# Kernel tuning notes

Hardware: AMD Instinct MI355X
Metric: run time of the kernel (lower is better)

## Reference

```python
import jax, jax.numpy as jnp
import numpy as np

B, N = 8, 4096
SEM_IN, SEM_OUT = 128, 13
INS_IN, INS_OUT = 128, 5
K = 30


def conv1x1(x, W, b):
    # x: [B, Cin, N], W: [Cout, Cin] -> [B, Cout, N]
    return jnp.einsum('oc,bcn->bon', W, x) + b[None, :, None]


def setup_inputs() -> dict:
    key = jax.random.key(0)
    ks = jax.random.split(key, 6)
    rn = lambda i, shape: jax.random.normal(ks[i], shape, dtype=jnp.float32)
    return {
        'f_sem': rn(0, (B, SEM_IN, N)),
        'f_ins': rn(1, (B, INS_IN, N)),
        'W_adapt': rn(2, (INS_IN, SEM_IN)) * 0.05,
        'b_adapt': jnp.zeros((INS_IN,), jnp.float32),
        'gamma_adapt': jnp.ones((INS_IN,), jnp.float32),
        'beta_adapt': jnp.zeros((INS_IN,), jnp.float32),
        'W_ins': rn(3, (INS_OUT, INS_IN)) * 0.05,
        'b_ins': jnp.zeros((INS_OUT,), jnp.float32),
        'W_sem': rn(4, (SEM_OUT, SEM_IN)) * 0.05,
        'b_sem': jnp.zeros((SEM_OUT,), jnp.float32),
    }


def reference(f_sem, f_ins, W_adapt, b_adapt, gamma_adapt, beta_adapt,
              W_ins, b_ins, W_sem, b_sem):
    # adaptation MLP: Conv1d(1x1) -> eval-mode BN (per-channel affine) -> ReLU
    adapted = conv1x1(f_sem, W_adapt, b_adapt)
    adapted = jax.nn.relu(adapted * gamma_adapt[None, :, None] + beta_adapt[None, :, None])
    f_sins = f_ins + adapted                       # [B, INS_IN, N]
    e_ins = conv1x1(f_sins, W_ins, b_ins)          # [B, INS_OUT, N]; Dropout=identity (eval)

    # k_nearest_neighbors(e_ins, e_ins, K): squared euclidean + top-k smallest
    sq = jnp.sum(e_ins * e_ins, axis=1)            # [B, N]
    dots = jnp.einsum('bcn,bcm->bnm', e_ins, e_ins)  # [B, N, N]
    dist = sq[:, :, None] - 2.0 * dots + sq[:, None, :]
    _, nn_idx = jax.lax.top_k(-dist, K)            # [B, N, K] indices of K nearest

    # index2points gather: [B, C, N, K]
    k_f_sem = jax.vmap(lambda f, i: f[:, i])(f_sem, nn_idx)
    f_isem = jnp.max(k_f_sem, axis=3)              # max over neighbors -> [B, C, N]

    p_sem = conv1x1(f_isem, W_sem, b_sem)          # [B, SEM_OUT, N]
    return p_sem, e_ins
```

## Files before the change

### kernel.cpp

```cpp
#include <hip/hip_runtime.h>
#include <stdint.h>

#define B_ 8
#define N_ 4096
#define C_ 128
#define OSEM 13
#define OINS 5
#define KNN 30
#define NSC 32
#define ROWS 4

typedef unsigned short u16;
typedef unsigned int u32;
typedef unsigned long long u64;

__device__ __forceinline__ float bf2f(u16 v) {
  u32 u = ((u32)v) << 16;
  return __uint_as_float(u);
}
__device__ __forceinline__ u16 f2bf(float f) {
  u32 u = __float_as_uint(f);
  u32 r = (u + 0x7FFFu + ((u >> 16) & 1u)) >> 16;
  return (u16)r;
}
__device__ __forceinline__ u32 monof(float d) {
  u32 u = __float_as_uint(d);
  return (u & 0x80000000u) ? ~u : (u | 0x80000000u);
}
__device__ __forceinline__ float unmonof(u32 p) {
  u32 u = (p & 0x80000000u) ? (p & 0x7FFFFFFFu) : ~p;
  return __uint_as_float(u);
}
__device__ __forceinline__ u64 monod(double d) {
  u64 u = (u64)__double_as_longlong(d);
  return (u & 0x8000000000000000ull) ? ~u : (u | 0x8000000000000000ull);
}
__device__ __forceinline__ int mbcnt64(u64 m) {
  return __builtin_amdgcn_mbcnt_hi((u32)(m >> 32),
                                   __builtin_amdgcn_mbcnt_lo((u32)m, 0));
}
__device__ __forceinline__ float rflf(float x) {
  return __uint_as_float(
      (u32)__builtin_amdgcn_readfirstlane((int)__float_as_uint(x)));
}

template <int M>
__device__ __forceinline__ float ldv(const void* p, size_t i) {
  if (M == 0) return bf2f(((const u16*)p)[i]);
  return ((const float*)p)[i];
}
template <int M>
__device__ __forceinline__ double ldvd(const void* p, size_t i) {
  return (double)ldv<M>(p, i);
}
template <int M>
__device__ __forceinline__ void stv(void* p, size_t i, float v) {
  if (M == 0) ((u16*)p)[i] = f2bf(v);
  else ((float*)p)[i] = v;
}
template <int M>
__device__ __forceinline__ void ld8(const void* p, size_t i, float* o) {
  if (M == 0) {
    uint4 u = *(const uint4*)((const u16*)p + i);
    o[0] = __uint_as_float(u.x << 16); o[1] = __uint_as_float(u.x & 0xFFFF0000u);
    o[2] = __uint_as_float(u.y << 16); o[3] = __uint_as_float(u.y & 0xFFFF0000u);
    o[4] = __uint_as_float(u.z << 16); o[5] = __uint_as_float(u.z & 0xFFFF0000u);
    o[6] = __uint_as_float(u.w << 16); o[7] = __uint_as_float(u.w & 0xFFFF0000u);
  } else {
    const float4* f = (const float4*)((const float*)p + i);
    float4 a = f[0], b = f[1];
    o[0] = a.x; o[1] = a.y; o[2] = a.z; o[3] = a.w;
    o[4] = b.x; o[5] = b.y; o[6] = b.z; o[7] = b.w;
  }
}

template <typename T>
__device__ __forceinline__ void transpose_body(const void* src_, void* dst_,
                                               char* tsm, int b, int c0,
                                               int n0) {
  T* t = (T*)tsm;
  const T* src0 = (const T*)src_;
  T* dst0 = (T*)dst_;
  int tid = threadIdx.x, j = tid & 63, i0 = tid >> 6;
  const T* src = src0 + (size_t)(b * C_ + c0) * N_ + n0;
#pragma unroll
  for (int k = 0; k < 16; ++k) {
    int i = k * 4 + i0;
    t[i * 65 + j] = src[(size_t)i * N_ + j];
  }
  __syncthreads();
  T* dst = dst0 + ((size_t)b * N_ + n0) * C_ + c0;
#pragma unroll
  for (int k = 0; k < 16; ++k) {
    int nl = k * 4 + i0;
    dst[(size_t)nl * C_ + j] = t[j * 65 + nl];
  }
}

template <int M>
__device__ void fused_body(const void* fsem, const void* fins, const void* Wad,
                           const void* bad, const void* gad, const void* bead,
                           const void* Wins, const void* bins,
                           float* __restrict__ q32, double* __restrict__ q64,
                           void* oute, char* smem, int b, int n0) {
  double* xs = (double*)smem;
  double* wt = (double*)(smem + 20480);
  float* fsh = (float*)smem;
  float* fsl = (float*)(smem + 32768);

  int tid = threadIdx.x, tx = tid & 7, ty = tid >> 3;

  double acc[4][8];
#pragma unroll
  for (int i = 0; i < 4; ++i)
#pragma unroll
    for (int j = 0; j < 8; ++j) acc[i][j] = 0.0;

  for (int kk = 0; kk < 128; kk += 32) {
    __syncthreads();
    {
      int r = tid >> 3, c8 = tid & 7;
      float v[8];
      ld8<M>(fsem, (size_t)(b * C_ + kk + r) * N_ + n0 + c8 * 8, v);
#pragma unroll
      for (int j = 0; j < 8; ++j) xs[r * 80 + c8 * 10 + j] = (double)v[j];
    }
#pragma unroll
    for (int it = 0; it < 16; ++it) {
      int f = it * 256 + tid;
      int k = f >> 7, c = f & 127;
      wt[k * 128 + c] = ldvd<M>(Wad, (size_t)c * C_ + kk + k);
    }
    __syncthreads();
#pragma unroll 2
    for (int k = 0; k < 32; ++k) {
      double xv[8], wv[4];
#pragma unroll
      for (int j = 0; j < 8; ++j) xv[j] = xs[k * 80 + tx * 10 + j];
#pragma unroll
      for (int i = 0; i < 4; ++i) wv[i] = wt[k * 128 + ty * 4 + i];
#pragma unroll
      for (int i = 0; i < 4; ++i)
#pragma unroll
        for (int j = 0; j < 8; ++j) acc[i][j] = fma(wv[i], xv[j], acc[i][j]);
    }
  }

#pragma unroll
  for (int i = 0; i < 4; ++i) {
    int c = ty * 4 + i;
    double ba = ldvd<M>(bad, c), ga = ldvd<M>(gad, c), be = ldvd<M>(bead, c);
    float ff[8];
    ld8<M>(fins, (size_t)(b * C_ + c) * N_ + n0 + tx * 8, ff);
#pragma unroll
    for (int j = 0; j < 8; ++j) {
      double a = acc[i][j] + ba;
      double h = a * ga + be;
      h = h > 0.0 ? h : 0.0;
      acc[i][j] = (double)ff[j] + h;
    }
  }
  __syncthreads();

#pragma unroll
  for (int i = 0; i < 4; ++i) {
    int c = ty * 4 + i;
#pragma unroll
    for (int j = 0; j < 8; ++j) {
      double fs = acc[i][j];
      float hi = (float)fs;
      fsh[c * 64 + tx * 8 + j] = hi;
      fsl[c * 64 + tx * 8 + j] = (float)(fs - (double)hi);
    }
  }
  __syncthreads();
  if (tid < 64) {
    int n = n0 + tid;
    double e[5] = {0.0, 0.0, 0.0, 0.0, 0.0};
#pragma unroll 4
    for (int c = 0; c < 128; ++c) {
      double fs = (double)fsh[c * 64 + tid] + (double)fsl[c * 64 + tid];
#pragma unroll
      for (int o = 0; o < 5; ++o)
        e[o] = fma(ldvd<M>(Wins, (size_t)o * C_ + c), fs, e[o]);
    }
    double sq = 0.0;
#pragma unroll
    for (int o = 0; o < 5; ++o) {
      e[o] = e[o] + ldvd<M>(bins, o);
      sq = fma(e[o], e[o], sq);
      stv<M>(oute, (size_t)(b * OINS + o) * N_ + n, (float)e[o]);
    }
    size_t row = (size_t)b * N_ + n;
    float* qp = q32 + row * 8;
    qp[0] = (float)e[0]; qp[1] = (float)e[1]; qp[2] = (float)e[2];
    qp[3] = (float)e[3]; qp[4] = (float)e[4]; qp[5] = (float)sq;
    qp[6] = 0.f; qp[7] = 0.f;
    double* qd = q64 + row * 8;
    qd[0] = e[0]; qd[1] = e[1]; qd[2] = e[2]; qd[3] = e[3]; qd[4] = e[4];
    qd[5] = sq; qd[6] = 0.0; qd[7] = 0.0;
  }
}

__global__ __launch_bounds__(256) void k_prep(
    const void* fsem, const void* fins, const void* Wad, const void* bad,
    const void* gad, const void* bead, const void* Wins, const void* bins,
    float* q32, double* q64, void* oute_bf, void* oute_f, void* fT,
    int useFT0, int useFT1, u32* flag) {
  __shared__ __align__(16) char smem[65536];
  __shared__ int sred[4];

  int tid = threadIdx.x;
  int csn = 0;
  {
    const u16* p = (const u16*)fsem;
#pragma unroll
    for (int i = 0; i < 4; ++i) {
      u16 v = p[2 * (tid * 4 + i)];
      u32 e = (v >> 7) & 0xFF;
      csn += (e >= 0x60 && e <= 0x9F) ? 1 : 0;
    }
#pragma unroll
    for (int s = 1; s < 64; s <<= 1) csn += __shfl_xor(csn, s, 64);
    if ((tid & 63) == 0) sred[tid >> 6] = csn;
  }
  __syncthreads();
  u32 fl = ((sred[0] + sred[1] + sred[2] + sred[3]) >= 614) ? 0u : 1u;

  int bx = blockIdx.x;
  if (bx == 0 && tid == 0) flag[0] = fl;

  if (bx < 512) {
    int b = bx >> 6, n0 = (bx & 63) * 64;
    if (fl == 0)
      fused_body<0>(fsem, fins, Wad, bad, gad, bead, Wins, bins, q32, q64,
                    oute_bf, smem, b, n0);
    else
      fused_body<1>(fsem, fins, Wad, bad, gad, bead, Wins, bins, q32, q64,
                    oute_f, smem, b, n0);
  } else {
    int idx = bx - 512;
    int n0 = (idx & 63) * 64, c0 = ((idx >> 6) & 1) * 64, b = idx >> 7;
    if (fl == 0) {
      if (!useFT0) return;
      transpose_body<u16>(fsem, fT, smem, b, c0, n0);
    } else {
      if (!useFT1) return;
      transpose_body<float>(fsem, fT, smem, b, c0, n0);
    }
  }
}

template <int M>
__device__ __forceinline__ void gather_pass(int b, const u32* __restrict__ fp,
                                            const void* fT, int c0,
                                            float* mx) {
#pragma unroll 3
  for (int k = 0; k < KNN; ++k) {
    int id = (int)fp[k];
    if (M == 0) {
      uint2 v = *(const uint2*)((const u16*)fT + (size_t)(b * N_ + id) * C_ + c0);
      mx[0] = fmaxf(mx[0], __uint_as_float(v.x << 16));
      mx[1] = fmaxf(mx[1], __uint_as_float(v.x & 0xFFFF0000u));
      mx[2] = fmaxf(mx[2], __uint_as_float(v.y << 16));
      mx[3] = fmaxf(mx[3], __uint_as_float(v.y & 0xFFFF0000u));
    } else {
      float4 v = *(const float4*)((const float*)fT + (size_t)(b * N_ + id) * C_ + c0);
      mx[0] = fmaxf(mx[0], v.x);
      mx[1] = fmaxf(mx[1], v.y);
      mx[2] = fmaxf(mx[2], v.z);
      mx[3] = fmaxf(mx[3], v.w);
    }
  }
}

template <int M>
__device__ __forceinline__ void gather_proj(int b, int n, const u32* fin,
                                            const void* fsem,
                                            const float* wsm,
                                            const float* bsm, float* fls,
                                            void* outv, int lane) {
  float mx0 = -__builtin_inff(), mx1 = -__builtin_inff();
  int c0 = lane * 2;
  size_t base = ((size_t)b * C_ + c0) * N_;
#pragma unroll 2
  for (int k = 0; k < KNN; ++k) {
    int id = (int)fin[k];
    mx0 = fmaxf(mx0, ldv<M>(fsem, base + id));
    mx1 = fmaxf(mx1, ldv<M>(fsem, base + N_ + id));
  }
  int g0 = c0 >> 5, cc0 = c0 & 31;
  fls[g0 * 33 + cc0] = mx0;
  fls[g0 * 33 + cc0 + 1] = mx1;
  if (lane < 52) {
    int o = lane >> 2, g = lane & 3;
    const float* wr = &wsm[(o * 4 + g) * 33];
    const float* fr = &fls[g * 33];
    float s = 0.f;
#pragma unroll
    for (int c = 0; c < 32; ++c) s = fmaf(wr[c], fr[c], s);
    s += __shfl_xor(s, 1, 64);
    s += __shfl_xor(s, 2, 64);
    if (g == 0) stv<M>(outv, ((size_t)b * OSEM + o) * N_ + n, s + bsm[o]);
  }
}

__global__ __launch_bounds__(256) void k_knn_out(
    const u32* flag, const float* __restrict__ q32,
    const double* __restrict__ q64, const void* fsem, const void* fT,
    int useFT0, int useFT1, const void* Wsem, const void* bsem, void* outv) {
  __shared__ u64 bufs[4][ROWS][128];
  __shared__ u32 idq[4][NSC];
  __shared__ u32 fin[4][ROWS][32];
  __shared__ float bsm[16];

  int tid = threadIdx.x, wid = tid >> 6, lane = tid & 63;
  u32 fl = *flag;
  int useFT = fl == 0 ? useFT0 : useFT1;

  int gw = blockIdx.x * 4 + wid;
  int b = gw >> 10;
  int r0 = (gw & 1023) * ROWS;
  const float* qb = q32 + (((size_t)b) << 12) * 8;
  u64(*buf)[128] = bufs[wid];

#pragma unroll
  for (int i = 0; i < 2 * ROWS; ++i) bufs[wid][0][i * 64 + lane] = ~0ull;

  float er2[ROWS][5], t[ROWS];
  int cnt[ROWS];
#pragma unroll
  for (int r = 0; r < ROWS; ++r) {
    const float* qr = qb + (size_t)(r0 + r) * 8;
    er2[r][0] = -2.f * qr[0]; er2[r][1] = -2.f * qr[1];
    er2[r][2] = -2.f * qr[2]; er2[r][3] = -2.f * qr[3];
    er2[r][4] = -2.f * qr[4];
    cnt[r] = 0;
  }

  auto rank_compress = [&](u64* bufr) -> float {
    u64 k0 = bufr[lane], k1 = bufr[lane + 64];
    int f0 = 0, f1 = 0;
#pragma unroll 4
    for (int j = 0; j < 64; ++j) {
      ulonglong2 kk = *(const ulonglong2*)&bufr[2 * j];
      f0 += (kk.x < k0) ? 1 : 0;
      f0 += (kk.y < k0) ? 1 : 0;
      f1 += (kk.x < k1) ? 1 : 0;
      f1 += (kk.y < k1) ? 1 : 0;
    }
    bool h31 = (f0 == 31) || (f1 == 31);
    u64 who = __ballot(h31);
    u32 pk = (f0 == 31) ? (u32)(k0 >> 32) : (u32)(k1 >> 32);
    int src = (int)(__ffsll((long long)who) - 1);
    pk = (u32)__shfl((int)pk, src, 64);
    bufr[64 + lane] = ~0ull;
    if (f0 < 64) bufr[f0] = k0;
    if (f1 < 64) bufr[f1] = k1;
    return unmonof(pk);
  };

  float minv[ROWS];
#pragma unroll
  for (int r = 0; r < ROWS; ++r) minv[r] = __builtin_inff();
  int pcur = gw & 31;
  float4 A0, A1;
  float2 B0, B1;
  {
    const float* g = qb + (size_t)pcur * 1024 + lane * 8;
    A0 = *(const float4*)(g);       B0 = *(const float2*)(g + 4);
    A1 = *(const float4*)(g + 512); B1 = *(const float2*)(g + 516);
  }
#pragma unroll 1
  for (int it = 0; it < 32; ++it) {
#pragma unroll
    for (int r = 0; r < ROWS; ++r) {
      float dd = B0.y;
      dd = fmaf(er2[r][0], A0.x, dd);
      dd = fmaf(er2[r][1], A0.y, dd);
      dd = fmaf(er2[r][2], A0.z, dd);
      dd = fmaf(er2[r][3], A0.w, dd);
      dd = fmaf(er2[r][4], B0.x, dd);
      float ee = B1.y;
      ee = fmaf(er2[r][0], A1.x, ee);
      ee = fmaf(er2[r][1], A1.y, ee);
      ee = fmaf(er2[r][2], A1.z, ee);
      ee = fmaf(er2[r][3], A1.w, ee);
      ee = fmaf(er2[r][4], B1.x, ee);
      minv[r] = fminf(minv[r], fminf(dd, ee));
    }
    pcur = (pcur + 1) & 31;
    {
      const float* g = qb + (size_t)pcur * 1024 + lane * 8;
      A0 = *(const float4*)(g);       B0 = *(const float2*)(g + 4);
      A1 = *(const float4*)(g + 512); B1 = *(const float2*)(g + 516);
    }
  }

  {
    u64 KM[ROWS];
    int fr2[ROWS];
#pragma unroll
    for (int r = 0; r < ROWS; ++r) {
      KM[r] = ((u64)monof(minv[r]) << 6) | (u32)lane;
      buf[r][lane] = KM[r];
      fr2[r] = 0;
    }
#pragma unroll 2
    for (int j = 0; j < 32; ++j) {
#pragma unroll
      for (int r = 0; r < ROWS; ++r) {
        ulonglong2 kk = *(const ulonglong2*)&buf[r][2 * j];
        fr2[r] += (kk.x < KM[r]) ? 1 : 0;
        fr2[r] += (kk.y < KM[r]) ? 1 : 0;
      }
    }
#pragma unroll
    for (int r = 0; r < ROWS; ++r) {
      bool h = (fr2[r] == 31);
      u64 who = __ballot(h);
      int src = (int)(__ffsll((long long)who) - 1);
      u32 pk = (u32)(KM[r] >> 6);
      pk = (u32)__shfl((int)pk, src, 64);
      t[r] = rflf(unmonof(pk));
      buf[r][lane] = ~0ull;
    }
  }

  pcur = gw & 31;
  {
    const float* g = qb + (size_t)pcur * 1024 + lane * 8;
    A0 = *(const float4*)(g);       B0 = *(const float2*)(g + 4);
    A1 = *(const float4*)(g + 512); B1 = *(const float2*)(g + 516);
  }
#pragma unroll 1
  for (int it = 0; it < 32; ++it) {
    int mb = pcur * 128;
    float d0[ROWS], d1[ROWS];
    u64 h0[ROWS], h1[ROWS];
#pragma unroll
    for (int r = 0; r < ROWS; ++r) {
      float dd = B0.y;
      dd = fmaf(er2[r][0], A0.x, dd);
      dd = fmaf(er2[r][1], A0.y, dd);
      dd = fmaf(er2[r][2], A0.z, dd);
      dd = fmaf(er2[r][3], A0.w, dd);
      dd = fmaf(er2[r][4], B0.x, dd);
      d0[r] = dd;
      float ee = B1.y;
      ee = fmaf(er2[r][0], A1.x, ee);
      ee = fmaf(er2[r][1], A1.y, ee);
      ee = fmaf(er2[r][2], A1.z, ee);
      ee = fmaf(er2[r][3], A1.w, ee);
      ee = fmaf(er2[r][4], B1.x, ee);
      d1[r] = ee;
      h0[r] = __ballot(dd <= t[r]);
      h1[r] = __ballot(ee <= t[r]);
    }
    pcur = (pcur + 1) & 31;
    {
      const float* g = qb + (size_t)pcur * 1024 + lane * 8;
      A0 = *(const float4*)(g);       B0 = *(const float2*)(g + 4);
      A1 = *(const float4*)(g + 512); B1 = *(const float2*)(g + 516);
    }
#pragma unroll
    for (int r = 0; r < ROWS; ++r) {
      u64 a = h0[r], c = h1[r];
      int m0 = mb + lane, m1 = mb + 64 + lane;
      if (a | c) {
        int ha = __popcll(a), hc = __popcll(c);
        if (cnt[r] + ha + hc <= 128) {
          int oa = mbcnt64(a), oc = ha + mbcnt64(c);
          if (d0[r] <= t[r])
            buf[r][cnt[r] + oa] = ((u64)monof(d0[r]) << 32) | (u32)m0;
          if (d1[r] <= t[r])
            buf[r][cnt[r] + oc] = ((u64)monof(d1[r]) << 32) | (u32)m1;
          cnt[r] += ha + hc;
        } else {
          if (cnt[r] + ha > 128) {
            t[r] = rflf(rank_compress(&buf[r][0]));
            cnt[r] = 64;
            a = __ballot(d0[r] <= t[r]);
            ha = __popcll(a);
          }
          if (ha) {
            int oa = mbcnt64(a);
            if (d0[r] <= t[r])
              buf[r][cnt[r] + oa] = ((u64)monof(d0[r]) << 32) | (u32)m0;
            cnt[r] += ha;
          }
          u64 c2 = __ballot(d1[r] <= t[r]);
          int hc2 = __popcll(c2);
          if (cnt[r] + hc2 > 128) {
            t[r] = rflf(rank_compress(&buf[r][0]));
            cnt[r] = 64;
            c2 = __ballot(d1[r] <= t[r]);
            hc2 = __popcll(c2);
          }
          if (hc2) {
            int oc = mbcnt64(c2);
            if (d1[r] <= t[r])
              buf[r][cnt[r] + oc] = ((u64)monof(d1[r]) << 32) | (u32)m1;
            cnt[r] += hc2;
          }
        }
      }
    }
  }

  const double* qdb = q64 + (((size_t)b) << 12) * 8;
  {
    u64 K0[ROWS], K1[ROWS];
    int f0[ROWS], f1[ROWS];
    int cmax = 0;
#pragma unroll
    for (int r = 0; r < ROWS; ++r) {
      K0[r] = buf[r][lane];
      K1[r] = buf[r][lane + 64];
      f0[r] = 0; f1[r] = 0;
      cmax = cnt[r] > cmax ? cnt[r] : cmax;
    }
    int JJ = (cmax + 1) >> 1;
#pragma unroll 2
    for (int j = 0; j < JJ; ++j) {
#pragma unroll
      for (int r = 0; r < ROWS; ++r) {
        ulonglong2 kk = *(const ulonglong2*)&buf[r][2 * j];
        f0[r] += (kk.x < K0[r]) ? 1 : 0;
        f0[r] += (kk.y < K0[r]) ? 1 : 0;
        f1[r] += (kk.x < K1[r]) ? 1 : 0;
        f1[r] += (kk.y < K1[r]) ? 1 : 0;
      }
    }
#pragma unroll 1
    for (int r = 0; r < ROWS; ++r) {
      if (f0[r] < NSC) idq[wid][f0[r]] = (u32)K0[r] & (N_ - 1);
      if (f1[r] < NSC) idq[wid][f1[r]] = (u32)K1[r] & (N_ - 1);

      const double* qdr = qdb + (size_t)(r0 + r) * 8;
      double D0 = qdr[0], D1 = qdr[1], D2 = qdr[2], D3 = qdr[3], D4 = qdr[4],
             DS = qdr[5];
      u64 key = ~0ull;
      u32 myid = 0;
      if (lane < NSC) {
        myid = idq[wid][lane];
        const double* qm = qdb + (size_t)myid * 8;
        double dot = D0 * qm[0];
        dot = fma(D1, qm[1], dot);
        dot = fma(D2, qm[2], dot);
        dot = fma(D3, qm[3], dot);
        dot = fma(D4, qm[4], dot);
        double dd = (DS - 2.0 * dot) + qm[5];
        key = (monod(dd) & ~0xFFFull) | myid;
      }
      buf[r][lane] = key;
      int rank = 0;
#pragma unroll
      for (int j = 0; j < NSC / 2; ++j) {
        ulonglong2 kk = *(const ulonglong2*)&buf[r][2 * j];
        rank += (kk.x < key) ? 1 : 0;
        rank += (kk.y < key) ? 1 : 0;
      }
      if (lane < NSC && rank < KNN) fin[wid][r][rank] = myid;
    }
  }

  __syncthreads();
  float* wsm = (float*)&bufs[0][0][0];
  float* flsb = (float*)&bufs[0][0][0] + 1728;
  for (int i = tid; i < 13 * 128; i += 256) {
    int o = i >> 7, cc = i & 127;
    wsm[(o * 4 + (cc >> 5)) * 33 + (cc & 31)] =
        (fl == 0) ? ldv<0>(Wsem, i) : ldv<1>(Wsem, i);
  }
  if (tid < OSEM) bsm[tid] = (fl == 0) ? ldv<0>(bsem, tid) : ldv<1>(bsem, tid);
  __syncthreads();

  if (useFT) {
    int h = lane >> 5, l5 = lane & 31, c0 = l5 * 4;
#pragma unroll 1
    for (int pass = 0; pass < 2; ++pass) {
      int r = pass * 2 + h;
      float mx[4] = {-__builtin_inff(), -__builtin_inff(), -__builtin_inff(),
                     -__builtin_inff()};
      if (fl == 0)
        gather_pass<0>(b, &fin[wid][r][0], fT, c0, mx);
      else
        gather_pass<1>(b, &fin[wid][r][0], fT, c0, mx);
      float* fr = flsb + (wid * ROWS + r) * 136 + (c0 >> 5) * 33 + (c0 & 31);
      fr[0] = mx[0]; fr[1] = mx[1]; fr[2] = mx[2]; fr[3] = mx[3];
    }
    if (lane < 52) {
      int o = lane >> 2, g = lane & 3;
      const float* wr = &wsm[(o * 4 + g) * 33];
      const float* p0 = flsb + (wid * ROWS + 0) * 136 + g * 33;
      const float* p1 = flsb + (wid * ROWS + 1) * 136 + g * 33;
      const float* p2 = flsb + (wid * ROWS + 2) * 136 + g * 33;
      const float* p3 = flsb + (wid * ROWS + 3) * 136 + g * 33;
      float s0 = 0.f, s1 = 0.f, s2 = 0.f, s3 = 0.f;
#pragma unroll
      for (int c = 0; c < 32; ++c) {
        float w = wr[c];
        s0 = fmaf(w, p0[c], s0);
        s1 = fmaf(w, p1[c], s1);
        s2 = fmaf(w, p2[c], s2);
        s3 = fmaf(w, p3[c], s3);
      }
      s0 += __shfl_xor(s0, 1, 64); s0 += __shfl_xor(s0, 2, 64);
      s1 += __shfl_xor(s1, 1, 64); s1 += __shfl_xor(s1, 2, 64);
      s2 += __shfl_xor(s2, 1, 64); s2 += __shfl_xor(s2, 2, 64);
      s3 += __shfl_xor(s3, 1, 64); s3 += __shfl_xor(s3, 2, 64);
      if (g == 0) {
        size_t ob = (size_t)b * OSEM + o;
        if (fl == 0) {
          stv<0>(outv, ob * N_ + r0 + 0, s0 + bsm[o]);
          stv<0>(outv, ob * N_ + r0 + 1, s1 + bsm[o]);
          stv<0>(outv, ob * N_ + r0 + 2, s2 + bsm[o]);
          stv<0>(outv, ob * N_ + r0 + 3, s3 + bsm[o]);
        } else {
          stv<1>(outv, ob * N_ + r0 + 0, s0 + bsm[o]);
          stv<1>(outv, ob * N_ + r0 + 1, s1 + bsm[o]);
          stv<1>(outv, ob * N_ + r0 + 2, s2 + bsm[o]);
          stv<1>(outv, ob * N_ + r0 + 3, s3 + bsm[o]);
        }
      }
    }
  } else {
    float* fls = flsb + (wid * ROWS) * 136;
#pragma unroll 1
    for (int r = 0; r < ROWS; ++r) {
      if (fl == 0)
        gather_proj<0>(b, r0 + r, &fin[wid][r][0], fsem, wsm, bsm, fls, outv,
                       lane);
      else
        gather_proj<1>(b, r0 + r, &fin[wid][r][0], fsem, wsm, bsm, fls, outv,
                       lane);
    }
  }
}

extern "C" void kernel_launch(void* const* d_in, const int* in_sizes, int n_in,
                              void* d_out, int out_size, void* d_ws,
                              size_t ws_size, hipStream_t stream) {
  (void)in_sizes; (void)n_in; (void)out_size;
  const void* fsem = d_in[0];
  const void* fins = d_in[1];
  const void* Wad = d_in[2];
  const void* bad = d_in[3];
  const void* gad = d_in[4];
  const void* bead = d_in[5];
  const void* Wins = d_in[6];
  const void* bins = d_in[7];
  const void* Wsem = d_in[8];
  const void* bsem = d_in[9];

  char* ws = (char*)d_ws;
  u32* flag = (u32*)ws;
  float* q32 = (float*)(ws + (1 << 20));
  double* q64 = (double*)(ws + (2 << 20));
  void* fT = (void*)(ws + (4 << 20));
  int useFT0 = (ws_size >= (size_t)(13 << 20)) ? 1 : 0;
  int useFT1 = (ws_size >= (size_t)(21 << 20)) ? 1 : 0;

  void* oute_bf = (void*)((u16*)d_out + (size_t)B_ * OSEM * N_);
  void* oute_f32 = (void*)((float*)d_out + (size_t)B_ * OSEM * N_);

  k_prep<<<dim3(1536), 256, 0, stream>>>(fsem, fins, Wad, bad, gad, bead,
                                         Wins, bins, q32, q64, oute_bf,
                                         oute_f32, fT, useFT0, useFT1, flag);
  k_knn_out<<<dim3(2048), 256, 0, stream>>>(flag, q32, q64, fsem, fT, useFT0,
                                            useFT1, Wsem, bsem, d_out);
}
```

Baseline: 259.6 us.

## Halve prep tile width, store adapt operands as float, parallelize e_ins projection

The fused prep kernel now processes 32 points per block instead of 64, doubling the fused-block count. The adapt-conv operands are staged in shared memory as float instead of double, and the accumulator shrinks from 4x8 to 2x8 doubles per thread. Shared memory drops from 64KB to about 34KB, which should raise occupancy and cut LDS traffic. The 5-output e_ins projection is split across 160 threads, one output channel each, instead of 64 threads computing all five. The cost is more blocks, an extra barrier, and more redundant weight loads per block.

```diff
diff --git a/kernel.cpp b/kernel.cpp
--- a/kernel.cpp
+++ b/kernel.cpp
@@ -73,6 +73,19 @@
     o[4] = b.x; o[5] = b.y; o[6] = b.z; o[7] = b.w;
   }
 }
+template <int M>
+__device__ __forceinline__ void ld4(const void* p, size_t i, float* o) {
+  if (M == 0) {
+    uint2 u = *(const uint2*)((const u16*)p + i);
+    o[0] = __uint_as_float(u.x << 16); o[1] = __uint_as_float(u.x & 0xFFFF0000u);
+    o[2] = __uint_as_float(u.y << 16); o[3] = __uint_as_float(u.y & 0xFFFF0000u);
+  } else {
+    float4 v = *(const float4*)((const float*)p + i);
+    o[0] = v.x; o[1] = v.y; o[2] = v.z; o[3] = v.w;
+  }
+}
+
+#define PREP_SMEM 34048
 
 template <typename T>
 __device__ __forceinline__ void transpose_body(const void* src_, void* dst_,
@@ -103,52 +116,55 @@
                            const void* Wins, const void* bins,
                            float* __restrict__ q32, double* __restrict__ q64,
                            void* oute, char* smem, int b, int n0) {
-  double* xs = (double*)smem;
-  double* wt = (double*)(smem + 20480);
+  float* wtf = (float*)smem;
+  float* xsf = (float*)(smem + 16384);
   float* fsh = (float*)smem;
-  float* fsl = (float*)(smem + 32768);
-
-  int tid = threadIdx.x, tx = tid & 7, ty = tid >> 3;
-
-  double acc[4][8];
-#pragma unroll
-  for (int i = 0; i < 4; ++i)
+  float* fsl = (float*)(smem + 16384);
+  double* est = (double*)(smem + 32768);
+
+  int tid = threadIdx.x, tx = tid & 3, ty = tid >> 2;
+
+  double acc[2][8];
+#pragma unroll
+  for (int i = 0; i < 2; ++i)
 #pragma unroll
     for (int j = 0; j < 8; ++j) acc[i][j] = 0.0;
 
   for (int kk = 0; kk < 128; kk += 32) {
     __syncthreads();
     {
-      int r = tid >> 3, c8 = tid & 7;
-      float v[8];
-      ld8<M>(fsem, (size_t)(b * C_ + kk + r) * N_ + n0 + c8 * 8, v);
-#pragma unroll
-      for (int j = 0; j < 8; ++j) xs[r * 80 + c8 * 10 + j] = (double)v[j];
+      int idx = tid * 4;
+      int k = idx >> 5, nn = idx & 31;
+      float v[4];
+      ld4<M>(fsem, (size_t)(b * C_ + kk + k) * N_ + n0 + nn, v);
+      xsf[k * 32 + nn] = v[0]; xsf[k * 32 + nn + 1] = v[1];
+      xsf[k * 32 + nn + 2] = v[2]; xsf[k * 32 + nn + 3] = v[3];
     }
 #pragma unroll
     for (int it = 0; it < 16; ++it) {
       int f = it * 256 + tid;
       int k = f >> 7, c = f & 127;
-      wt[k * 128 + c] = ldvd<M>(Wad, (size_t)c * C_ + kk + k);
+      wtf[k * 128 + c] = ldv<M>(Wad, (size_t)c * C_ + kk + k);
     }
     __syncthreads();
 #pragma unroll 2
     for (int k = 0; k < 32; ++k) {
-      double xv[8], wv[4];
-#pragma unroll
-      for (int j = 0; j < 8; ++j) xv[j] = xs[k * 80 + tx * 10 + j];
-#pragma unroll
-      for (int i = 0; i < 4; ++i) wv[i] = wt[k * 128 + ty * 4 + i];
-#pragma unroll
-      for (int i = 0; i < 4; ++i)
-#pragma unroll
-        for (int j = 0; j < 8; ++j) acc[i][j] = fma(wv[i], xv[j], acc[i][j]);
-    }
-  }
-
-#pragma unroll
-  for (int i = 0; i < 4; ++i) {
-    int c = ty * 4 + i;
+      float xvf[8], wvf[2];
+#pragma unroll
+      for (int j = 0; j < 8; ++j) xvf[j] = xsf[k * 32 + tx * 8 + j];
+#pragma unroll
+      for (int i = 0; i < 2; ++i) wvf[i] = wtf[k * 128 + ty * 2 + i];
+#pragma unroll
+      for (int i = 0; i < 2; ++i)
+#pragma unroll
+        for (int j = 0; j < 8; ++j)
+          acc[i][j] = fma((double)wvf[i], (double)xvf[j], acc[i][j]);
+    }
+  }
+
+#pragma unroll
+  for (int i = 0; i < 2; ++i) {
+    int c = ty * 2 + i;
     double ba = ldvd<M>(bad, c), ga = ldvd<M>(gad, c), be = ldvd<M>(bead, c);
     float ff[8];
     ld8<M>(fins, (size_t)(b * C_ + c) * N_ + n0 + tx * 8, ff);
@@ -163,31 +179,39 @@
   __syncthreads();
 
 #pragma unroll
-  for (int i = 0; i < 4; ++i) {
-    int c = ty * 4 + i;
+  for (int i = 0; i < 2; ++i) {
+    int c = ty * 2 + i;
 #pragma unroll
     for (int j = 0; j < 8; ++j) {
       double fs = acc[i][j];
       float hi = (float)fs;
-      fsh[c * 64 + tx * 8 + j] = hi;
-      fsl[c * 64 + tx * 8 + j] = (float)(fs - (double)hi);
+      fsh[c * 32 + tx * 8 + j] = hi;
+      fsl[c * 32 + tx * 8 + j] = (float)(fs - (double)hi);
     }
   }
   __syncthreads();
-  if (tid < 64) {
+  {
+    int lane = tid & 63;
+    int slot = (tid >> 6) * 2 + (lane >> 5);
+    int n = lane & 31;
+    if (slot < 5) {
+      double e = 0.0;
+#pragma unroll 4
+      for (int c = 0; c < 128; ++c) {
+        double fs = (double)fsh[c * 32 + n] + (double)fsl[c * 32 + n];
+        e = fma(ldvd<M>(Wins, (size_t)slot * C_ + c), fs, e);
+      }
+      est[slot * 32 + n] = e;
+    }
+  }
+  __syncthreads();
+  if (tid < 32) {
     int n = n0 + tid;
-    double e[5] = {0.0, 0.0, 0.0, 0.0, 0.0};
-#pragma unroll 4
-    for (int c = 0; c < 128; ++c) {
-      double fs = (double)fsh[c * 64 + tid] + (double)fsl[c * 64 + tid];
-#pragma unroll
-      for (int o = 0; o < 5; ++o)
-        e[o] = fma(ldvd<M>(Wins, (size_t)o * C_ + c), fs, e[o]);
-    }
+    double e[5];
     double sq = 0.0;
 #pragma unroll
     for (int o = 0; o < 5; ++o) {
-      e[o] = e[o] + ldvd<M>(bins, o);
+      e[o] = est[o * 32 + tid] + ldvd<M>(bins, o);
       sq = fma(e[o], e[o], sq);
       stv<M>(oute, (size_t)(b * OINS + o) * N_ + n, (float)e[o]);
     }
@@ -207,7 +231,7 @@
     const void* gad, const void* bead, const void* Wins, const void* bins,
     float* q32, double* q64, void* oute_bf, void* oute_f, void* fT,
     int useFT0, int useFT1, u32* flag) {
-  __shared__ __align__(16) char smem[65536];
+  __shared__ __align__(16) char smem[PREP_SMEM];
   __shared__ int sred[4];
 
   int tid = threadIdx.x;
@@ -230,8 +254,8 @@
   int bx = blockIdx.x;
   if (bx == 0 && tid == 0) flag[0] = fl;
 
-  if (bx < 512) {
-    int b = bx >> 6, n0 = (bx & 63) * 64;
+  if (bx < 1024) {
+    int b = bx >> 7, n0 = (bx & 127) * 32;
     if (fl == 0)
       fused_body<0>(fsem, fins, Wad, bad, gad, bead, Wins, bins, q32, q64,
                     oute_bf, smem, b, n0);
@@ -239,7 +263,7 @@
       fused_body<1>(fsem, fins, Wad, bad, gad, bead, Wins, bins, q32, q64,
                     oute_f, smem, b, n0);
   } else {
-    int idx = bx - 512;
+    int idx = bx - 1024;
     int n0 = (idx & 63) * 64, c0 = ((idx >> 6) & 1) * 64, b = idx >> 7;
     if (fl == 0) {
       if (!useFT0) return;
@@ -665,7 +689,7 @@
   void* oute_bf = (void*)((u16*)d_out + (size_t)B_ * OSEM * N_);
   void* oute_f32 = (void*)((float*)d_out + (size_t)B_ * OSEM * N_);
 
-  k_prep<<<dim3(1536), 256, 0, stream>>>(fsem, fins, Wad, bad, gad, bead,
+  k_prep<<<dim3(2048), 256, 0, stream>>>(fsem, fins, Wad, bad, gad, bead,
                                          Wins, bins, q32, q64, oute_bf,
                                          oute_f32, fT, useFT0, useFT1, flag);
   k_knn_out<<<dim3(2048), 256, 0, stream>>>(flag, q32, q64, fsem, fT, useFT0,
```

Measured after the change: 276.4 us. +6.5%, slower.

## Swizzle block-to-row mapping and scan candidates sequentially without staggered prefetch

Applied to the files above, without the earlier changes.

Block indices are remapped so consecutive blocks land on different batches, spreading concurrent waves across batches and possibly across caches. The staggered per-wave start offset (gw&31) and its software prefetch are replaced by a plain sequential scan from column zero. The first min pass is unrolled to four column groups per iteration, issuing more loads at once. This gives up the staggering that spread waves across different L2 lines and the explicit load-ahead, in exchange for simpler addressing and more loads in flight per iteration.

```diff
diff --git a/kernel.cpp b/kernel.cpp
--- a/kernel.cpp
+++ b/kernel.cpp
@@ -318,7 +318,9 @@
   u32 fl = *flag;
   int useFT = fl == 0 ? useFT0 : useFT1;
 
-  int gw = blockIdx.x * 4 + wid;
+  int bid = blockIdx.x;
+  int swz = ((bid & 7) << 8) | (bid >> 3);
+  int gw = swz * 4 + wid;
   int b = gw >> 10;
   int r0 = (gw & 1023) * ROWS;
   const float* qb = q32 + (((size_t)b) << 12) * 8;
@@ -360,40 +362,38 @@
     return unmonof(pk);
   };
 
+#define DIST(dst, X, Y, r)                      \
+  {                                             \
+    float dd_ = (Y).y;                          \
+    dd_ = fmaf(er2[r][0], (X).x, dd_);          \
+    dd_ = fmaf(er2[r][1], (X).y, dd_);          \
+    dd_ = fmaf(er2[r][2], (X).z, dd_);          \
+    dd_ = fmaf(er2[r][3], (X).w, dd_);          \
+    dd_ = fmaf(er2[r][4], (Y).x, dd_);          \
+    (dst) = dd_;                                \
+  }
+
   float minv[ROWS];
 #pragma unroll
   for (int r = 0; r < ROWS; ++r) minv[r] = __builtin_inff();
-  int pcur = gw & 31;
-  float4 A0, A1;
-  float2 B0, B1;
   {
-    const float* g = qb + (size_t)pcur * 1024 + lane * 8;
-    A0 = *(const float4*)(g);       B0 = *(const float2*)(g + 4);
-    A1 = *(const float4*)(g + 512); B1 = *(const float2*)(g + 516);
-  }
+    const float* g = qb + lane * 8;
 #pragma unroll 1
-  for (int it = 0; it < 32; ++it) {
-#pragma unroll
-    for (int r = 0; r < ROWS; ++r) {
-      float dd = B0.y;
-      dd = fmaf(er2[r][0], A0.x, dd);
-      dd = fmaf(er2[r][1], A0.y, dd);
-      dd = fmaf(er2[r][2], A0.z, dd);
-      dd = fmaf(er2[r][3], A0.w, dd);
-      dd = fmaf(er2[r][4], B0.x, dd);
-      float ee = B1.y;
-      ee = fmaf(er2[r][0], A1.x, ee);
-      ee = fmaf(er2[r][1], A1.y, ee);
-      ee = fmaf(er2[r][2], A1.z, ee);
-      ee = fmaf(er2[r][3], A1.w, ee);
-      ee = fmaf(er2[r][4], B1.x, ee);
-      minv[r] = fminf(minv[r], fminf(dd, ee));
-    }
-    pcur = (pcur + 1) & 31;
-    {
-      const float* g = qb + (size_t)pcur * 1024 + lane * 8;
-      A0 = *(const float4*)(g);       B0 = *(const float2*)(g + 4);
-      A1 = *(const float4*)(g + 512); B1 = *(const float2*)(g + 516);
+    for (int it = 0; it < 16; ++it) {
+      float4 Aa = *(const float4*)(g);        float2 Ba = *(const float2*)(g + 4);
+      float4 Ab = *(const float4*)(g + 512);  float2 Bb = *(const float2*)(g + 516);
+      float4 Ac = *(const float4*)(g + 1024); float2 Bc = *(const float2*)(g + 1028);
+      float4 Ad = *(const float4*)(g + 1536); float2 Bd = *(const float2*)(g + 1540);
+      g += 2048;
+#pragma unroll
+      for (int r = 0; r < ROWS; ++r) {
+        float da, db, dc, dd;
+        DIST(da, Aa, Ba, r);
+        DIST(db, Ab, Bb, r);
+        DIST(dc, Ac, Bc, r);
+        DIST(dd, Ad, Bd, r);
+        minv[r] = fminf(minv[r], fminf(fminf(da, db), fminf(dc, dd)));
+      }
     }
   }
 
@@ -427,86 +427,70 @@
     }
   }
 
-  pcur = gw & 31;
   {
-    const float* g = qb + (size_t)pcur * 1024 + lane * 8;
-    A0 = *(const float4*)(g);       B0 = *(const float2*)(g + 4);
-    A1 = *(const float4*)(g + 512); B1 = *(const float2*)(g + 516);
-  }
+    const float* g = qb + lane * 8;
+    int mbase = 0;
 #pragma unroll 1
-  for (int it = 0; it < 32; ++it) {
-    int mb = pcur * 128;
-    float d0[ROWS], d1[ROWS];
-    u64 h0[ROWS], h1[ROWS];
-#pragma unroll
-    for (int r = 0; r < ROWS; ++r) {
-      float dd = B0.y;
-      dd = fmaf(er2[r][0], A0.x, dd);
-      dd = fmaf(er2[r][1], A0.y, dd);
-      dd = fmaf(er2[r][2], A0.z, dd);
-      dd = fmaf(er2[r][3], A0.w, dd);
-      dd = fmaf(er2[r][4], B0.x, dd);
-      d0[r] = dd;
-      float ee = B1.y;
-      ee = fmaf(er2[r][0], A1.x, ee);
-      ee = fmaf(er2[r][1], A1.y, ee);
-      ee = fmaf(er2[r][2], A1.z, ee);
-      ee = fmaf(er2[r][3], A1.w, ee);
-      ee = fmaf(er2[r][4], B1.x, ee);
-      d1[r] = ee;
-      h0[r] = __ballot(dd <= t[r]);
-      h1[r] = __ballot(ee <= t[r]);
-    }
-    pcur = (pcur + 1) & 31;
-    {
-      const float* g = qb + (size_t)pcur * 1024 + lane * 8;
-      A0 = *(const float4*)(g);       B0 = *(const float2*)(g + 4);
-      A1 = *(const float4*)(g + 512); B1 = *(const float2*)(g + 516);
-    }
-#pragma unroll
-    for (int r = 0; r < ROWS; ++r) {
-      u64 a = h0[r], c = h1[r];
-      int m0 = mb + lane, m1 = mb + 64 + lane;
-      if (a | c) {
-        int ha = __popcll(a), hc = __popcll(c);
-        if (cnt[r] + ha + hc <= 128) {
-          int oa = mbcnt64(a), oc = ha + mbcnt64(c);
-          if (d0[r] <= t[r])
-            buf[r][cnt[r] + oa] = ((u64)monof(d0[r]) << 32) | (u32)m0;
-          if (d1[r] <= t[r])
-            buf[r][cnt[r] + oc] = ((u64)monof(d1[r]) << 32) | (u32)m1;
-          cnt[r] += ha + hc;
-        } else {
-          if (cnt[r] + ha > 128) {
-            t[r] = rflf(rank_compress(&buf[r][0]));
-            cnt[r] = 64;
-            a = __ballot(d0[r] <= t[r]);
-            ha = __popcll(a);
-          }
-          if (ha) {
-            int oa = mbcnt64(a);
+    for (int it = 0; it < 32; ++it) {
+      float4 A0 = *(const float4*)(g);       float2 B0 = *(const float2*)(g + 4);
+      float4 A1 = *(const float4*)(g + 512); float2 B1 = *(const float2*)(g + 516);
+      g += 1024;
+      float d0[ROWS], d1[ROWS];
+      u64 h0[ROWS], h1[ROWS];
+#pragma unroll
+      for (int r = 0; r < ROWS; ++r) {
+        DIST(d0[r], A0, B0, r);
+        DIST(d1[r], A1, B1, r);
+        h0[r] = __ballot(d0[r] <= t[r]);
+        h1[r] = __ballot(d1[r] <= t[r]);
+      }
+#pragma unroll
+      for (int r = 0; r < ROWS; ++r) {
+        u64 a = h0[r], c = h1[r];
+        int m0 = mbase + lane, m1 = mbase + 64 + lane;
+        if (a | c) {
+          int ha = __popcll(a), hc = __popcll(c);
+          if (cnt[r] + ha + hc <= 128) {
+            int oa = mbcnt64(a), oc = ha + mbcnt64(c);
             if (d0[r] <= t[r])
               buf[r][cnt[r] + oa] = ((u64)monof(d0[r]) << 32) | (u32)m0;
-            cnt[r] += ha;
-          }
-          u64 c2 = __ballot(d1[r] <= t[r]);
-          int hc2 = __popcll(c2);
-          if (cnt[r] + hc2 > 128) {
-            t[r] = rflf(rank_compress(&buf[r][0]));
-            cnt[r] = 64;
-            c2 = __ballot(d1[r] <= t[r]);
-            hc2 = __popcll(c2);
-          }
-          if (hc2) {
-            int oc = mbcnt64(c2);
             if (d1[r] <= t[r])
               buf[r][cnt[r] + oc] = ((u64)monof(d1[r]) << 32) | (u32)m1;
-            cnt[r] += hc2;
+            cnt[r] += ha + hc;
+          } else {
+            if (cnt[r] + ha > 128) {
+              t[r] = rflf(rank_compress(&buf[r][0]));
+              cnt[r] = 64;
+              a = __ballot(d0[r] <= t[r]);
+              ha = __popcll(a);
+            }
+            if (ha) {
+              int oa = mbcnt64(a);
+              if (d0[r] <= t[r])
+                buf[r][cnt[r] + oa] = ((u64)monof(d0[r]) << 32) | (u32)m0;
+              cnt[r] += ha;
+            }
+            u64 c2 = __ballot(d1[r] <= t[r]);
+            int hc2 = __popcll(c2);
+            if (cnt[r] + hc2 > 128) {
+              t[r] = rflf(rank_compress(&buf[r][0]));
+              cnt[r] = 64;
+              c2 = __ballot(d1[r] <= t[r]);
+              hc2 = __popcll(c2);
+            }
+            if (hc2) {
+              int oc = mbcnt64(c2);
+              if (d1[r] <= t[r])
+                buf[r][cnt[r] + oc] = ((u64)monof(d1[r]) << 32) | (u32)m1;
+              cnt[r] += hc2;
+            }
           }
         }
       }
-    }
-  }
+      mbase += 128;
+    }
+  }
+#undef DIST
 
   const double* qdb = q64 + (((size_t)b) << 12) * 8;
   {
```

Measured after the change: 254.6 us. About the same (-1.9%).
